# Optimization experiments

Measured on AMD Instinct MI355X. Metric: run time of the kernel, lower is better.

Reference implementation:

```python
import jax, jax.numpy as jnp
import numpy as np

N = 50000      # nodes
E = 800000     # edges
F_IN = 128     # input_channels
H = 128        # hidden_channels
OUT = 10       # output_channels
G = 64         # graphs in batch


def setup_inputs() -> dict:
    key = jax.random.key(0)
    ks = jax.random.split(key, 16)
    s = 0.05
    inp = {
        "x": jax.random.normal(ks[0], (N, F_IN), jnp.float32),
        "edge_index": jax.random.randint(ks[1], (2, E), 0, N, jnp.int64 if jax.config.jax_enable_x64 else jnp.int32),
        "batch": jnp.sort(jax.random.randint(ks[2], (N,), 0, G, jnp.int32)),
        "conv1_w": jax.random.normal(ks[3], (F_IN, H), jnp.float32) * s,
        "conv1_b": jnp.zeros((H,), jnp.float32),
        "conv2_w": jax.random.normal(ks[4], (H, H), jnp.float32) * s,
        "conv2_b": jnp.zeros((H,), jnp.float32),
        "conv3_w": jax.random.normal(ks[5], (H, H), jnp.float32) * s,
        "conv3_b": jnp.zeros((H,), jnp.float32),
        "fc1_w": jax.random.normal(ks[6], (H, 8 * H), jnp.float32) * s,
        "fc1_b": jnp.zeros((8 * H,), jnp.float32),
        "fc2_w": jax.random.normal(ks[7], (8 * H, 4 * H), jnp.float32) * s,
        "fc2_b": jnp.zeros((4 * H,), jnp.float32),
        "fc3_w": jax.random.normal(ks[8], (4 * H, 2 * H), jnp.float32) * s,
        "fc3_b": jnp.zeros((2 * H,), jnp.float32),
        "fc4_w": jax.random.normal(ks[9], (2 * H, H), jnp.float32) * s,
        "fc4_b": jnp.zeros((H,), jnp.float32),
        "fc5_w": jax.random.normal(ks[10], (H, OUT), jnp.float32) * s,
        "fc5_b": jnp.zeros((OUT,), jnp.float32),
    }
    return inp


def _gcn_conv(x, w, b, src, dst, norm, n_nodes):
    # GCNConv: out = D^{-1/2} (A + I) D^{-1/2} X W + b   (self-loops already in src/dst)
    xw = x @ w                                        # [N, H]
    msg = xw[src] * norm[:, None]                     # gather + scale, [E+N, H]
    return jax.ops.segment_sum(msg, dst, num_segments=n_nodes) + b


def reference(x, edge_index, batch,
              conv1_w, conv1_b, conv2_w, conv2_b, conv3_w, conv3_b,
              fc1_w, fc1_b, fc2_w, fc2_b, fc3_w, fc3_b,
              fc4_w, fc4_b, fc5_w, fc5_b):
    n = x.shape[0]
    loop = jnp.arange(n, dtype=edge_index.dtype)
    src = jnp.concatenate([edge_index[0], loop])      # add self-loops
    dst = jnp.concatenate([edge_index[1], loop])
    deg = jax.ops.segment_sum(jnp.ones_like(dst, dtype=x.dtype), dst, num_segments=n)
    dinv = jnp.where(deg > 0, jax.lax.rsqrt(deg), 0.0)
    norm = dinv[src] * dinv[dst]                      # symmetric normalization per edge

    h = jax.nn.relu(_gcn_conv(x, conv1_w, conv1_b, src, dst, norm, n))
    h = jax.nn.relu(_gcn_conv(h, conv2_w, conv2_b, src, dst, norm, n))
    h = _gcn_conv(h, conv3_w, conv3_b, src, dst, norm, n)

    # global mean pool over graphs
    sums = jax.ops.segment_sum(h, batch, num_segments=G)
    cnt = jax.ops.segment_sum(jnp.ones((n,), x.dtype), batch, num_segments=G)
    f = sums / jnp.maximum(cnt, 1.0)[:, None]         # [G, H]

    y = jax.nn.relu(f @ fc1_w + fc1_b)
    y = jax.nn.relu(y @ fc2_w + fc2_b)
    y = jax.nn.relu(y @ fc3_w + fc3_b)
    y = jax.nn.relu(y @ fc4_w + fc4_b)
    # dropout p=0.5 is identity in eval mode
    y = y @ fc5_w + fc5_b                             # [G, OUT]
    return (f, y)
```

## Files before the change

### kernel.cpp

```cpp
#include <hip/hip_runtime.h>
#include <stdint.h>

#define N_NODES 50000
#define N_EDGES 800000
#define N_PAD   50176
#define PCHUNK  512
#define NCHUNKS 98
#define FEAT    128
#define NGRAPH  64

#define E_BLKS      3125
#define GSTRIP_BLKS 782
#define GR_BLKS     (GSTRIP_BLKS + E_BLKS)
#define CZ_BLKS     3136

typedef __attribute__((ext_vector_type(8))) short short8;
typedef __attribute__((ext_vector_type(4))) float floatx4;

static __device__ __forceinline__ ushort f2bf(float f) {
  uint32_t x = __float_as_uint(f);
  x += 0x7FFF + ((x >> 16) & 1);
  return (ushort)(x >> 16);
}
static __device__ __forceinline__ float bfLo(uint32_t u) {
  return __uint_as_float(u << 16);
}
static __device__ __forceinline__ float bfHi(uint32_t u) {
  return __uint_as_float(u & 0xFFFF0000u);
}

static __device__ __forceinline__ void cvt4T(const float* __restrict__ in,
                                             ushort* __restrict__ outT, int i) {
  float4 v = ((const float4*)in)[i];
  int k = (4 * i) >> 7;
  int n = (4 * i) & 127;
  outT[(size_t)(n + 0) * FEAT + k] = f2bf(v.x);
  outT[(size_t)(n + 1) * FEAT + k] = f2bf(v.y);
  outT[(size_t)(n + 2) * FEAT + k] = f2bf(v.z);
  outT[(size_t)(n + 3) * FEAT + k] = f2bf(v.w);
}

__global__ __launch_bounds__(256) void wcvt(const float* __restrict__ w0,
                                            const float* __restrict__ w1,
                                            ushort* __restrict__ wbT) {
  int i = blockIdx.x * 256 + threadIdx.x;
  if (i < 4096) cvt4T(w0, wbT, i);
  else cvt4T(w1, wbT + FEAT * FEAT, i - 4096);
}

static __device__ __forceinline__ void gemm_strip_f32a(int strip, int lane,
                                                       const float* __restrict__ X,
                                                       const ushort* __restrict__ WT,
                                                       ushort* __restrict__ XW) {
  if (strip >= N_NODES / 16) return;
  int m0 = strip * 16;
  int r = lane & 15, quad = lane >> 4;
  const float* xrow = X + (size_t)(m0 + r) * FEAT;
  short8 afr[4];
#pragma unroll
  for (int kb = 0; kb < 4; ++kb) {
    int k0 = kb * 32 + quad * 8;
    float4 f0 = *(const float4*)(xrow + k0);
    float4 f1 = *(const float4*)(xrow + k0 + 4);
    short8 a;
    a[0] = (short)f2bf(f0.x); a[1] = (short)f2bf(f0.y);
    a[2] = (short)f2bf(f0.z); a[3] = (short)f2bf(f0.w);
    a[4] = (short)f2bf(f1.x); a[5] = (short)f2bf(f1.y);
    a[6] = (short)f2bf(f1.z); a[7] = (short)f2bf(f1.w);
    afr[kb] = a;
  }
#pragma unroll
  for (int nt = 0; nt < 8; ++nt) {
    int n0 = nt * 16;
    floatx4 acc = {0.f, 0.f, 0.f, 0.f};
    const ushort* wrow = WT + (size_t)(n0 + r) * FEAT;
#pragma unroll
    for (int kb = 0; kb < 4; ++kb) {
      short8 b = *(const short8*)(wrow + kb * 32 + quad * 8);
      acc = __builtin_amdgcn_mfma_f32_16x16x32_bf16(afr[kb], b, acc, 0, 0, 0);
    }
#pragma unroll
    for (int reg = 0; reg < 4; ++reg)
      XW[(size_t)(m0 + quad * 4 + reg) * FEAT + n0 + r] = f2bf(acc[reg]);
  }
}

__global__ __launch_bounds__(256) void gemm_rank(const float* __restrict__ x,
                                                 const ushort* __restrict__ wbT,
                                                 ushort* __restrict__ msl,
                                                 const int* __restrict__ dst,
                                                 int* __restrict__ cnt_p,
                                                 int* __restrict__ rank,
                                                 float* __restrict__ coefT) {
  int b = blockIdx.x, t = threadIdx.x;
  if (b < GR_BLKS) {
    int fifth = b / 5;
    if (b - fifth * 5 == 0) {
      gemm_strip_f32a(fifth * 4 + (t >> 6), t & 63, x, wbT, msl);
    } else {
      int e = (b - fifth - 1) * 256 + t;
      rank[e] = atomicAdd(&cnt_p[dst[e] * 8], 1);
    }
  } else {
    int i = (b - GR_BLKS) * 256 + t;
    ((float4*)coefT)[i] = make_float4(0.f, 0.f, 0.f, 0.f);
  }
}

__global__ __launch_bounds__(256) void gemm2_strip(const ushort* __restrict__ X,
                                                   const ushort* __restrict__ WT,
                                                   ushort* __restrict__ XW) {
  int strip = (blockIdx.x * 256 + threadIdx.x) >> 6;
  int lane = threadIdx.x & 63;
  if (strip >= N_NODES / 16) return;
  int m0 = strip * 16;
  int r = lane & 15, quad = lane >> 4;
  const ushort* xrow = X + (size_t)(m0 + r) * FEAT;
  short8 afr[4];
#pragma unroll
  for (int kb = 0; kb < 4; ++kb)
    afr[kb] = *(const short8*)(xrow + kb * 32 + quad * 8);
#pragma unroll
  for (int nt = 0; nt < 8; ++nt) {
    int n0 = nt * 16;
    floatx4 acc = {0.f, 0.f, 0.f, 0.f};
    const ushort* wrow = WT + (size_t)(n0 + r) * FEAT;
#pragma unroll
    for (int kb = 0; kb < 4; ++kb) {
      short8 b = *(const short8*)(wrow + kb * 32 + quad * 8);
      acc = __builtin_amdgcn_mfma_f32_16x16x32_bf16(afr[kb], b, acc, 0, 0, 0);
    }
#pragma unroll
    for (int reg = 0; reg < 4; ++reg)
      XW[(size_t)(m0 + quad * 4 + reg) * FEAT + n0 + r] = f2bf(acc[reg]);
  }
}

__global__ __launch_bounds__(256) void dinv_scan1(const int* __restrict__ cnt_p,
                                                  const int* __restrict__ batch,
                                                  float* __restrict__ dinv,
                                                  float* __restrict__ cnt_g,
                                                  int* __restrict__ ptr,
                                                  int* __restrict__ bsums,
                                                  float* __restrict__ coefT) {
  __shared__ int tmp[256];
  __shared__ int bins[NGRAPH];
  if (threadIdx.x < NGRAPH) bins[threadIdx.x] = 0;
  int i = blockIdx.x * 256 + threadIdx.x;
  int v = (i < N_NODES) ? cnt_p[i * 8] : 0;
  tmp[threadIdx.x] = v;
  __syncthreads();
  for (int off = 1; off < 256; off <<= 1) {
    int t = (threadIdx.x >= off) ? tmp[threadIdx.x - off] : 0;
    __syncthreads();
    tmp[threadIdx.x] += t;
    __syncthreads();
  }
  if (i < N_NODES) ptr[i] = tmp[threadIdx.x] - v;
  if (threadIdx.x == 255) bsums[blockIdx.x] = tmp[255];
  if (i < N_NODES) {
    float di = rsqrtf((float)v + 1.0f);
    dinv[i] = di;
    int g = batch[i];
    coefT[(size_t)g * N_PAD + i] = di * di;
    atomicAdd(&bins[g], 1);
  }
  __syncthreads();
  if (threadIdx.x < NGRAPH && bins[threadIdx.x] > 0)
    atomicAdd(&cnt_g[threadIdx.x], (float)bins[threadIdx.x]);
}

__global__ __launch_bounds__(256) void scan2(int* __restrict__ bsums, int nb) {
  __shared__ int tmp[256];
  int v = (threadIdx.x < nb) ? bsums[threadIdx.x] : 0;
  tmp[threadIdx.x] = v;
  __syncthreads();
  for (int off = 1; off < 256; off <<= 1) {
    int t = (threadIdx.x >= off) ? tmp[threadIdx.x - off] : 0;
    __syncthreads();
    tmp[threadIdx.x] += t;
    __syncthreads();
  }
  if (threadIdx.x < nb) bsums[threadIdx.x] = tmp[threadIdx.x] - v;
}

__global__ __launch_bounds__(256) void scan3(int* __restrict__ ptr,
                                             const int* __restrict__ bsums) {
  int i = blockIdx.x * 256 + threadIdx.x;
  if (i < N_NODES) ptr[i] += bsums[blockIdx.x];
}

__global__ __launch_bounds__(256) void fill_csr(const int* __restrict__ src,
                                                const int* __restrict__ dst,
                                                const int* __restrict__ rank,
                                                const int* __restrict__ ptr,
                                                const float* __restrict__ dinv,
                                                const int* __restrict__ batch,
                                                int2* __restrict__ edges,
                                                float* __restrict__ coefT) {
  int e = blockIdx.x * 256 + threadIdx.x;
  if (e >= N_EDGES) return;
  int s = src[e];
  int d = dst[e];
  float ds = dinv[s];
  edges[ptr[d] + rank[e]] = make_int2(s, __float_as_int(ds));
  atomicAdd(&coefT[(size_t)batch[d] * N_PAD + s], ds * dinv[d]);
}

static __device__ __forceinline__ float2 agg_node(const uint32_t* __restrict__ m32,
                                                  const int2* __restrict__ edges,
                                                  int start, int n, int lane) {
  float ax0 = 0.f, ay0 = 0.f, ax1 = 0.f, ay1 = 0.f;
  float ax2 = 0.f, ay2 = 0.f, ax3 = 0.f, ay3 = 0.f;
  int i = 0;
  if ((start & 1) && n > 0) {
    int2 e = edges[start];
    uint32_t u = m32[(size_t)e.x * 64 + lane];
    float nrm = __int_as_float(e.y);
    ax0 = fmaf(nrm, bfLo(u), ax0);
    ay0 = fmaf(nrm, bfHi(u), ay0);
    i = 1;
  }
  for (; i + 8 <= n; i += 8) {
    const int4* ep = (const int4*)(edges + start + i);
    int4 q0 = ep[0], q1 = ep[1], q2 = ep[2], q3 = ep[3];
    uint32_t u0 = m32[(size_t)q0.x * 64 + lane];
    uint32_t u1 = m32[(size_t)q0.z * 64 + lane];
    uint32_t u2 = m32[(size_t)q1.x * 64 + lane];
    uint32_t u3 = m32[(size_t)q1.z * 64 + lane];
    uint32_t u4 = m32[(size_t)q2.x * 64 + lane];
    uint32_t u5 = m32[(size_t)q2.z * 64 + lane];
    uint32_t u6 = m32[(size_t)q3.x * 64 + lane];
    uint32_t u7 = m32[(size_t)q3.z * 64 + lane];
    float n0 = __int_as_float(q0.y), n1 = __int_as_float(q0.w);
    float n2 = __int_as_float(q1.y), n3 = __int_as_float(q1.w);
    float n4 = __int_as_float(q2.y), n5 = __int_as_float(q2.w);
    float n6 = __int_as_float(q3.y), n7 = __int_as_float(q3.w);
    ax0 = fmaf(n0, bfLo(u0), ax0); ay0 = fmaf(n0, bfHi(u0), ay0);
    ax1 = fmaf(n1, bfLo(u1), ax1); ay1 = fmaf(n1, bfHi(u1), ay1);
    ax2 = fmaf(n2, bfLo(u2), ax2); ay2 = fmaf(n2, bfHi(u2), ay2);
    ax3 = fmaf(n3, bfLo(u3), ax3); ay3 = fmaf(n3, bfHi(u3), ay3);
    ax0 = fmaf(n4, bfLo(u4), ax0); ay0 = fmaf(n4, bfHi(u4), ay0);
    ax1 = fmaf(n5, bfLo(u5), ax1); ay1 = fmaf(n5, bfHi(u5), ay1);
    ax2 = fmaf(n6, bfLo(u6), ax2); ay2 = fmaf(n6, bfHi(u6), ay2);
    ax3 = fmaf(n7, bfLo(u7), ax3); ay3 = fmaf(n7, bfHi(u7), ay3);
  }
  for (; i < n; ++i) {
    int2 e = edges[start + i];
    float nrm = __int_as_float(e.y);
    uint32_t u = m32[(size_t)e.x * 64 + lane];
    ax0 = fmaf(nrm, bfLo(u), ax0);
    ay0 = fmaf(nrm, bfHi(u), ay0);
  }
  return make_float2((ax0 + ax1) + (ax2 + ax3), (ay0 + ay1) + (ay2 + ay3));
}

__global__ __launch_bounds__(256) void agg_kernel(const ushort* __restrict__ msg,
                                                  const float* __restrict__ dinv,
                                                  const int* __restrict__ ptr,
                                                  const int* __restrict__ cnt_p,
                                                  const int2* __restrict__ edges,
                                                  const float* __restrict__ bias,
                                                  ushort* __restrict__ outp) {
  int wave = (blockIdx.x * 256 + threadIdx.x) >> 6;
  int lane = threadIdx.x & 63;
  if (wave >= N_NODES) return;
  int v = wave;
  float di = dinv[v];
  const uint32_t* m32 = (const uint32_t*)msg;
  uint32_t su = m32[(size_t)v * 64 + lane];
  float2 s = agg_node(m32, edges, ptr[v], cnt_p[v * 8], lane);
  float ax = fmaf(fmaf(di, bfLo(su), s.x), di, bias[2 * lane]);
  float ay = fmaf(fmaf(di, bfHi(su), s.y), di, bias[2 * lane + 1]);
  ushort2 h2;
  h2.x = f2bf(fmaxf(ax, 0.f));
  h2.y = f2bf(fmaxf(ay, 0.f));
  ((ushort2*)outp)[(size_t)v * 64 + lane] = h2;
}

__global__ __launch_bounds__(512) void pool_mfma(const ushort* __restrict__ h2,
                                                 const float* __restrict__ coefT,
                                                 float* __restrict__ P) {
  __shared__ ushort cs[64 * PCHUNK];
  int t = threadIdx.x;
  int lane = t & 63;
  int w = t >> 6;
  int r = lane & 15, quad = lane >> 4;
  int n0 = w * 16;
  floatx4 acc[4];
#pragma unroll
  for (int mt = 0; mt < 4; ++mt) acc[mt] = (floatx4){0.f, 0.f, 0.f, 0.f};
#pragma unroll 1
  for (int cc = 0; cc < 2; ++cc) {
    int c0 = (blockIdx.x * 2 + cc) * PCHUNK;
#pragma unroll 4
    for (int it = 0; it < 16; ++it) {
      int f4 = t + it * 512;
      int g = f4 >> 7;
      int k = (f4 & 127) * 4;
      float4 v = *(const float4*)(coefT + (size_t)g * N_PAD + c0 + k);
      ushort4 u;
      u.x = f2bf(v.x); u.y = f2bf(v.y); u.z = f2bf(v.z); u.w = f2bf(v.w);
      uint32_t off = ((uint32_t)g * (PCHUNK * 2) + k * 2) ^ ((g & 7) << 4);
      *(ushort4*)((char*)cs + off) = u;
    }
    __syncthreads();
#pragma unroll 2
    for (int kb = 0; kb < 16; ++kb) {
      int k0c = kb * 32 + quad * 8;
      short8 bfr;
#pragma unroll
      for (int j = 0; j < 8; ++j)
        bfr[j] = (short)h2[(size_t)(c0 + k0c + j) * FEAT + n0 + r];
#pragma unroll
      for (int mt = 0; mt < 4; ++mt) {
        int row = mt * 16 + r;
        uint32_t off = ((uint32_t)row * (PCHUNK * 2) + k0c * 2) ^ ((row & 7) << 4);
        short8 a = *(const short8*)((const char*)cs + off);
        acc[mt] = __builtin_amdgcn_mfma_f32_16x16x32_bf16(a, bfr, acc[mt], 0, 0, 0);
      }
    }
    __syncthreads();
  }
#pragma unroll
  for (int mt = 0; mt < 4; ++mt)
#pragma unroll
    for (int reg = 0; reg < 4; ++reg)
      atomicAdd(&P[(size_t)(mt * 16 + quad * 4 + reg) * FEAT + n0 + r],
                acc[mt][reg]);
}

template <int K, int C, int KSLICE, int RELU_IN, int DIVC, int NSPLIT>
__global__ __launch_bounds__(256) void fc_layer(const float* __restrict__ IN,
                                                const float* __restrict__ W,
                                                const float* __restrict__ Bs,
                                                const float* __restrict__ cntg,
                                                float* __restrict__ OUT) {
  constexpr int CB = (C + 63) / 64;
  int lane = threadIdx.x & 63;
  int gq = threadIdx.x >> 6;
  int bid = blockIdx.x;
  int kp = bid % NSPLIT;
  int rest = bid / NSPLIT;
  int cg = rest % CB;
  int g = (rest / CB) * 4 + gq;
  int c = cg * 64 + lane;
  if (c >= C) return;
  int k0 = kp * KSLICE;
  const float* wp = W + (size_t)k0 * C + c;
  const float* in = IN + (size_t)g * K + k0;
  float cf = 1.f;
  if (DIVC) cf = fmaxf(cntg[g], 1.f);
  float a0 = 0.f, a1 = 0.f, a2 = 0.f, a3 = 0.f;
  float a4 = 0.f, a5 = 0.f, a6 = 0.f, a7 = 0.f;
#pragma unroll 2
  for (int k = 0; k < KSLICE; k += 8) {
    float i0 = in[k + 0], i1 = in[k + 1], i2 = in[k + 2], i3 = in[k + 3];
    float i4 = in[k + 4], i5 = in[k + 5], i6 = in[k + 6], i7 = in[k + 7];
    if (RELU_IN) {
      i0 = fmaxf(i0, 0.f); i1 = fmaxf(i1, 0.f);
      i2 = fmaxf(i2, 0.f); i3 = fmaxf(i3, 0.f);
      i4 = fmaxf(i4, 0.f); i5 = fmaxf(i5, 0.f);
      i6 = fmaxf(i6, 0.f); i7 = fmaxf(i7, 0.f);
    }
    if (DIVC) {
      i0 /= cf; i1 /= cf; i2 /= cf; i3 /= cf;
      i4 /= cf; i5 /= cf; i6 /= cf; i7 /= cf;
    }
    a0 = fmaf(i0, wp[(size_t)(k + 0) * C], a0);
    a1 = fmaf(i1, wp[(size_t)(k + 1) * C], a1);
    a2 = fmaf(i2, wp[(size_t)(k + 2) * C], a2);
    a3 = fmaf(i3, wp[(size_t)(k + 3) * C], a3);
    a4 = fmaf(i4, wp[(size_t)(k + 4) * C], a4);
    a5 = fmaf(i5, wp[(size_t)(k + 5) * C], a5);
    a6 = fmaf(i6, wp[(size_t)(k + 6) * C], a6);
    a7 = fmaf(i7, wp[(size_t)(k + 7) * C], a7);
  }
  float s = ((a0 + a1) + (a2 + a3)) + ((a4 + a5) + (a6 + a7));
  if (NSPLIT == 1) {
    OUT[(size_t)g * C + c] = s + Bs[c];
  } else {
    atomicAdd(&OUT[(size_t)g * C + c], s + (kp == 0 ? Bs[c] : 0.f));
  }
}

extern "C" void kernel_launch(void* const* d_in, const int* in_sizes, int n_in,
                              void* d_out, int out_size, void* d_ws, size_t ws_size,
                              hipStream_t stream) {
  const float* x         = (const float*)d_in[0];
  const int*   ei        = (const int*)d_in[1];
  const int*   batch     = (const int*)d_in[2];
  const float* conv_w[3] = {(const float*)d_in[3], (const float*)d_in[5], (const float*)d_in[7]};
  const float* conv_b[3] = {(const float*)d_in[4], (const float*)d_in[6], (const float*)d_in[8]};
  const float* fc_w[5]   = {(const float*)d_in[9],  (const float*)d_in[11],
                            (const float*)d_in[13], (const float*)d_in[15],
                            (const float*)d_in[17]};
  const float* fc_b[5]   = {(const float*)d_in[10], (const float*)d_in[12],
                            (const float*)d_in[14], (const float*)d_in[16],
                            (const float*)d_in[18]};
  const int* e_src = ei;
  const int* e_dst = ei + N_EDGES;
  float* out_f = (float*)d_out;
  float* out_y = (float*)d_out + NGRAPH * FEAT;

  char* p = (char*)d_ws;
  auto carve = [&](size_t bytes) {
    char* r = p;
    p += (bytes + 255) & ~(size_t)255;
    return r;
  };
  int*    cnt_p   = (int*)carve((size_t)N_NODES * 32);
  float*  dinv    = (float*)carve(N_NODES * 4);
  int*    csr_ptr = (int*)carve(N_NODES * 4);
  int*    bsums   = (int*)carve(256 * 4);
  int2*   edges   = (int2*)carve((size_t)N_EDGES * 8);
  ushort* wbT     = (ushort*)carve((size_t)2 * FEAT * FEAT * 2);
  ushort* hbuf    = (ushort*)carve((size_t)N_PAD * FEAT * 2);
  float*  coefT   = (float*)carve((size_t)NGRAPH * N_PAD * 4);
  float*  f_sum   = (float*)carve(NGRAPH * FEAT * 4);
  float*  cnt_g   = (float*)carve(NGRAPH * 4);
  float*  Y1      = (float*)carve(NGRAPH * 1024 * 4);
  float*  Y2      = (float*)carve(NGRAPH * 512 * 4);
  float*  Y3      = (float*)carve(NGRAPH * 256 * 4);
  float*  Y4      = (float*)carve(NGRAPH * 128 * 4);
  char*   region  = carve((size_t)N_EDGES * 4 + (size_t)N_NODES * FEAT * 2);
  int*    rank    = (int*)region;
  ushort* msl1    = (ushort*)(region + (size_t)N_EDGES * 4);
  ushort* msl2    = (ushort*)region;

  const int BLK_N = (N_NODES + 255) / 256;

  hipMemsetAsync(cnt_p, 0, (size_t)N_NODES * 32, stream);
  hipMemsetAsync(f_sum, 0, NGRAPH * FEAT * 4 + 256, stream);
  hipMemsetAsync(Y2, 0, NGRAPH * (512 + 256 + 128) * 4, stream);

  wcvt<<<32, 256, 0, stream>>>(conv_w[0], conv_w[1], wbT);

  gemm_rank<<<GR_BLKS + CZ_BLKS, 256, 0, stream>>>(x, wbT, msl1, e_dst, cnt_p,
                                                   rank, coefT);

  dinv_scan1<<<BLK_N, 256, 0, stream>>>(cnt_p, batch, dinv, cnt_g, csr_ptr,
                                        bsums, coefT);
  scan2<<<1, 256, 0, stream>>>(bsums, BLK_N);
  scan3<<<BLK_N, 256, 0, stream>>>(csr_ptr, bsums);

  fill_csr<<<E_BLKS, 256, 0, stream>>>(e_src, e_dst, rank, csr_ptr, dinv,
                                       batch, edges, coefT);

  const int AGG_BLKS = (N_NODES + 3) / 4;

  agg_kernel<<<AGG_BLKS, 256, 0, stream>>>(msl1, dinv, csr_ptr, cnt_p, edges,
                                           conv_b[0], hbuf);
  gemm2_strip<<<GSTRIP_BLKS, 256, 0, stream>>>(hbuf, wbT + FEAT * FEAT, msl2);
  agg_kernel<<<AGG_BLKS, 256, 0, stream>>>(msl2, dinv, csr_ptr, cnt_p, edges,
                                           conv_b[1], hbuf);
  pool_mfma<<<NCHUNKS / 2, 512, 0, stream>>>(hbuf, coefT, f_sum);

  fc_layer< 128, 128, 128, 0, 1, 1><<< 32, 256, 0, stream>>>(f_sum, conv_w[2], conv_b[2], cnt_g, out_f);
  fc_layer< 128,1024, 128, 0, 0, 1><<<256, 256, 0, stream>>>(out_f, fc_w[0], fc_b[0], nullptr, Y1);
  fc_layer<1024, 512, 256, 1, 0, 4><<<512, 256, 0, stream>>>(Y1, fc_w[1], fc_b[1], nullptr, Y2);
  fc_layer< 512, 256, 128, 1, 0, 4><<<256, 256, 0, stream>>>(Y2, fc_w[2], fc_b[2], nullptr, Y3);
  fc_layer< 256, 128,  32, 1, 0, 8><<<256, 256, 0, stream>>>(Y3, fc_w[3], fc_b[3], nullptr, Y4);
  fc_layer< 128,  10, 128, 1, 0, 1><<< 16, 256, 0, stream>>>(Y4, fc_w[4], fc_b[4], nullptr, out_y);
}
```

Measured before the change: 364.7 us.

## Move coefT zeroing to wcvt and coef atomics into first aggregation kernel

Zeroing of the pooling coefficient matrix moves from the gemm_rank launch into the weight-conversion kernel. The per-edge atomic accumulation into coefT moves out of fill_csr and into the first aggregation launch, interleaved one block in five. This shortens the critical fill_csr and gemm_rank kernels and overlaps the scattered atomics with the memory-bound gather. The risk is that the atomics contend with the aggregation for memory bandwidth, and dinv_scan1 still writes coefT after it is zeroed.

```diff
diff --git a/kernel.cpp b/kernel.cpp
--- a/kernel.cpp
+++ b/kernel.cpp
@@ -13,6 +13,7 @@
 #define GSTRIP_BLKS 782
 #define GR_BLKS     (GSTRIP_BLKS + E_BLKS)
 #define CZ_BLKS     3136
+#define AGG_BLKS    12500
 
 typedef __attribute__((ext_vector_type(8))) short short8;
 typedef __attribute__((ext_vector_type(4))) float floatx4;
@@ -42,10 +43,17 @@
 
 __global__ __launch_bounds__(256) void wcvt(const float* __restrict__ w0,
                                             const float* __restrict__ w1,
-                                            ushort* __restrict__ wbT) {
-  int i = blockIdx.x * 256 + threadIdx.x;
-  if (i < 4096) cvt4T(w0, wbT, i);
-  else cvt4T(w1, wbT + FEAT * FEAT, i - 4096);
+                                            ushort* __restrict__ wbT,
+                                            float* __restrict__ coefT) {
+  int b = blockIdx.x, t = threadIdx.x;
+  if (b < 32) {
+    int i = b * 256 + t;
+    if (i < 4096) cvt4T(w0, wbT, i);
+    else cvt4T(w1, wbT + FEAT * FEAT, i - 4096);
+  } else {
+    int i = (b - 32) * 256 + t;
+    ((float4*)coefT)[i] = make_float4(0.f, 0.f, 0.f, 0.f);
+  }
 }
 
 static __device__ __forceinline__ void gemm_strip_f32a(int strip, int lane,
@@ -90,20 +98,14 @@
                                                  ushort* __restrict__ msl,
                                                  const int* __restrict__ dst,
                                                  int* __restrict__ cnt_p,
-                                                 int* __restrict__ rank,
-                                                 float* __restrict__ coefT) {
+                                                 int* __restrict__ rank) {
   int b = blockIdx.x, t = threadIdx.x;
-  if (b < GR_BLKS) {
-    int fifth = b / 5;
-    if (b - fifth * 5 == 0) {
-      gemm_strip_f32a(fifth * 4 + (t >> 6), t & 63, x, wbT, msl);
-    } else {
-      int e = (b - fifth - 1) * 256 + t;
-      rank[e] = atomicAdd(&cnt_p[dst[e] * 8], 1);
-    }
+  int fifth = b / 5;
+  if (b - fifth * 5 == 0) {
+    gemm_strip_f32a(fifth * 4 + (t >> 6), t & 63, x, wbT, msl);
   } else {
-    int i = (b - GR_BLKS) * 256 + t;
-    ((float4*)coefT)[i] = make_float4(0.f, 0.f, 0.f, 0.f);
+    int e = (b - fifth - 1) * 256 + t;
+    rank[e] = atomicAdd(&cnt_p[dst[e] * 8], 1);
   }
 }
 
@@ -195,16 +197,11 @@
                                                 const int* __restrict__ rank,
                                                 const int* __restrict__ ptr,
                                                 const float* __restrict__ dinv,
-                                                const int* __restrict__ batch,
-                                                int2* __restrict__ edges,
-                                                float* __restrict__ coefT) {
+                                                int2* __restrict__ edges) {
   int e = blockIdx.x * 256 + threadIdx.x;
   if (e >= N_EDGES) return;
   int s = src[e];
-  int d = dst[e];
-  float ds = dinv[s];
-  edges[ptr[d] + rank[e]] = make_int2(s, __float_as_int(ds));
-  atomicAdd(&coefT[(size_t)batch[d] * N_PAD + s], ds * dinv[d]);
+  edges[ptr[dst[e]] + rank[e]] = make_int2(s, __float_as_int(dinv[s]));
 }
 
 static __device__ __forceinline__ float2 agg_node(const uint32_t* __restrict__ m32,
@@ -255,17 +252,14 @@
   return make_float2((ax0 + ax1) + (ax2 + ax3), (ay0 + ay1) + (ay2 + ay3));
 }
 
-__global__ __launch_bounds__(256) void agg_kernel(const ushort* __restrict__ msg,
-                                                  const float* __restrict__ dinv,
-                                                  const int* __restrict__ ptr,
-                                                  const int* __restrict__ cnt_p,
-                                                  const int2* __restrict__ edges,
-                                                  const float* __restrict__ bias,
-                                                  ushort* __restrict__ outp) {
-  int wave = (blockIdx.x * 256 + threadIdx.x) >> 6;
-  int lane = threadIdx.x & 63;
-  if (wave >= N_NODES) return;
-  int v = wave;
+static __device__ __forceinline__ void agg_one(int v, int lane,
+                                               const ushort* __restrict__ msg,
+                                               const float* __restrict__ dinv,
+                                               const int* __restrict__ ptr,
+                                               const int* __restrict__ cnt_p,
+                                               const int2* __restrict__ edges,
+                                               const float* __restrict__ bias,
+                                               ushort* __restrict__ outp) {
   float di = dinv[v];
   const uint32_t* m32 = (const uint32_t*)msg;
   uint32_t su = m32[(size_t)v * 64 + lane];
@@ -276,6 +270,42 @@
   h2.x = f2bf(fmaxf(ax, 0.f));
   h2.y = f2bf(fmaxf(ay, 0.f));
   ((ushort2*)outp)[(size_t)v * 64 + lane] = h2;
+}
+
+__global__ __launch_bounds__(256) void agg1_coef(const ushort* __restrict__ msg,
+                                                 const float* __restrict__ dinv,
+                                                 const int* __restrict__ ptr,
+                                                 const int* __restrict__ cnt_p,
+                                                 const int2* __restrict__ edges,
+                                                 const float* __restrict__ bias,
+                                                 ushort* __restrict__ outp,
+                                                 const int* __restrict__ src,
+                                                 const int* __restrict__ dst,
+                                                 const int* __restrict__ batch,
+                                                 float* __restrict__ coefT) {
+  int b = blockIdx.x, t = threadIdx.x;
+  int fifth = b / 5;
+  int rem = b - fifth * 5;
+  if (rem < 4) {
+    int ab = fifth * 4 + rem;
+    agg_one(ab * 4 + (t >> 6), t & 63, msg, dinv, ptr, cnt_p, edges, bias, outp);
+  } else {
+    int e = fifth * 256 + t;
+    int s = src[e], d = dst[e];
+    atomicAdd(&coefT[(size_t)batch[d] * N_PAD + s], dinv[s] * dinv[d]);
+  }
+}
+
+__global__ __launch_bounds__(256) void agg_kernel(const ushort* __restrict__ msg,
+                                                  const float* __restrict__ dinv,
+                                                  const int* __restrict__ ptr,
+                                                  const int* __restrict__ cnt_p,
+                                                  const int2* __restrict__ edges,
+                                                  const float* __restrict__ bias,
+                                                  ushort* __restrict__ outp) {
+  int wave = (blockIdx.x * 256 + threadIdx.x) >> 6;
+  if (wave >= N_NODES) return;
+  agg_one(wave, threadIdx.x & 63, msg, dinv, ptr, cnt_p, edges, bias, outp);
 }
 
 __global__ __launch_bounds__(512) void pool_mfma(const ushort* __restrict__ h2,
@@ -434,26 +464,23 @@
   hipMemsetAsync(f_sum, 0, NGRAPH * FEAT * 4 + 256, stream);
   hipMemsetAsync(Y2, 0, NGRAPH * (512 + 256 + 128) * 4, stream);
 
-  wcvt<<<32, 256, 0, stream>>>(conv_w[0], conv_w[1], wbT);
-
-  gemm_rank<<<GR_BLKS + CZ_BLKS, 256, 0, stream>>>(x, wbT, msl1, e_dst, cnt_p,
-                                                   rank, coefT);
+  wcvt<<<32 + CZ_BLKS, 256, 0, stream>>>(conv_w[0], conv_w[1], wbT, coefT);
+
+  gemm_rank<<<GR_BLKS, 256, 0, stream>>>(x, wbT, msl1, e_dst, cnt_p, rank);
 
   dinv_scan1<<<BLK_N, 256, 0, stream>>>(cnt_p, batch, dinv, cnt_g, csr_ptr,
                                         bsums, coefT);
   scan2<<<1, 256, 0, stream>>>(bsums, BLK_N);
   scan3<<<BLK_N, 256, 0, stream>>>(csr_ptr, bsums);
 
-  fill_csr<<<E_BLKS, 256, 0, stream>>>(e_src, e_dst, rank, csr_ptr, dinv,
-                                       batch, edges, coefT);
-
-  const int AGG_BLKS = (N_NODES + 3) / 4;
-
-  agg_kernel<<<AGG_BLKS, 256, 0, stream>>>(msl1, dinv, csr_ptr, cnt_p, edges,
-                                           conv_b[0], hbuf);
+  fill_csr<<<E_BLKS, 256, 0, stream>>>(e_src, e_dst, rank, csr_ptr, dinv, edges);
+
+  agg1_coef<<<AGG_BLKS + E_BLKS, 256, 0, stream>>>(
+      msl1, dinv, csr_ptr, cnt_p, edges, conv_b[0], hbuf,
+      e_src, e_dst, batch, coefT);
   gemm2_strip<<<GSTRIP_BLKS, 256, 0, stream>>>(hbuf, wbT + FEAT * FEAT, msl2);
-  agg_kernel<<<AGG_BLKS, 256, 0, stream>>>(msl2, dinv, csr_ptr, cnt_p, edges,
-                                           conv_b[1], hbuf);
+  agg_kernel<<<(N_NODES + 3) / 4, 256, 0, stream>>>(msl2, dinv, csr_ptr, cnt_p,
+                                                    edges, conv_b[1], hbuf);
   pool_mfma<<<NCHUNKS / 2, 512, 0, stream>>>(hbuf, coefT, f_sum);
 
   fc_layer< 128, 128, 128, 0, 1, 1><<< 32, 256, 0, stream>>>(f_sum, conv_w[2], conv_b[2], cnt_g, out_f);
```

New measurement: 348.3 us. 1.05x faster.
